# Optimization experiments

Measured on AMD Instinct MI355X. Metric: run time of the kernel, lower is better.

## Reference

```python
import jax, jax.numpy as jnp
import numpy as np

N_NODES = 100000
EPS = 1e-5


def gcn_conv(x, edge_index, W, b):
    # PyG GCNConv: add self loops, symmetric normalization, aggregate at target.
    n = x.shape[0]
    xw = x @ W                                  # [N, F_out]
    loop = jnp.arange(n)
    src = jnp.concatenate([edge_index[0], loop])
    dst = jnp.concatenate([edge_index[1], loop])
    deg = jax.ops.segment_sum(jnp.ones_like(dst, dtype=xw.dtype), dst, num_segments=n)
    dinv = jnp.where(deg > 0, jax.lax.rsqrt(deg), 0.0)
    norm = dinv[src] * dinv[dst]                # [E+N]
    out = jax.ops.segment_sum(norm[:, None] * xw[src], dst, num_segments=n)
    return out + b


def batch_norm(x, gamma, beta):
    # training-mode BatchNorm1d over node dim
    m = x.mean(axis=0)
    v = x.var(axis=0)
    return (x - m) * jax.lax.rsqrt(v + EPS) * gamma + beta


def setup_inputs() -> dict:
    key = jax.random.key(0)
    ks = jax.random.split(key, 16)
    dims = [(128, 256), (256, 128), (128, 64)]
    inp = {
        "x": jax.random.normal(ks[0], (N_NODES, 128), dtype=jnp.float32),
        "edge_index": jax.random.randint(ks[1], (2, 1600000), 0, N_NODES),
        "pos_edge_index": jax.random.randint(ks[2], (2, 200000), 0, N_NODES),
        "neg_edge_index": jax.random.randint(ks[3], (2, 200000), 0, N_NODES),
    }
    for i, (fi, fo) in enumerate(dims, start=1):
        inp[f"W{i}"] = jax.random.normal(ks[3 + i], (fi, fo), dtype=jnp.float32) / np.sqrt(fi)
        inp[f"b{i}"] = jnp.zeros((fo,), dtype=jnp.float32)
        inp[f"g{i}"] = jnp.ones((fo,), dtype=jnp.float32)
        inp[f"beta{i}"] = jnp.zeros((fo,), dtype=jnp.float32)
    return inp


def reference(x, edge_index, pos_edge_index, neg_edge_index,
              W1, b1, g1, beta1, W2, b2, g2, beta2, W3, b3, g3, beta3):
    # encode
    h = gcn_conv(x, edge_index, W1, b1)
    h = jax.nn.sigmoid(batch_norm(h, g1, beta1))
    h = gcn_conv(h, edge_index, W2, b2)
    h = jax.nn.sigmoid(batch_norm(h, g2, beta2))
    h = gcn_conv(h, edge_index, W3, b3)
    z = batch_norm(h, g3, beta3)                # [N, 64]
    # decode
    ei = jnp.concatenate([pos_edge_index, neg_edge_index], axis=-1)
    logits = jnp.sum(z[ei[0]] * z[ei[1]], axis=-1)
    return logits
```

## Files before the change

### kernel.cpp

```cpp
#include <hip/hip_runtime.h>
#include <hip/hip_bf16.h>
#include <stddef.h>


#define WAVE 64
#define BSHIFT 9
#define SCHUNK 4096

typedef __attribute__((ext_vector_type(8))) short short8;
typedef __attribute__((ext_vector_type(4))) float f32x4;

__device__ __forceinline__ float bl(uint g) { return __uint_as_float(g << 16); }
__device__ __forceinline__ float bh(uint g) { return __uint_as_float(g & 0xffff0000u); }
__device__ __forceinline__ ushort f2b(float f) {
    uint u = __float_as_uint(f);
    return (ushort)((u + 0x7fffu + ((u >> 16) & 1u)) >> 16);
}
__device__ __forceinline__ uint pack2(float lo, float hi) {
    return (uint)f2b(lo) | ((uint)f2b(hi) << 16);
}

__global__ __launch_bounds__(256) void k_bhist(const int* __restrict__ dst, int* __restrict__ gh, int E) {
    __shared__ int lh[256];
    lh[threadIdx.x] = 0; __syncthreads();
    int i = blockIdx.x * 256 + threadIdx.x, stride = gridDim.x * 256;
    for (; i < E; i += stride) atomicAdd(&lh[dst[i] >> BSHIFT], 1);
    __syncthreads();
    int v = lh[threadIdx.x];
    if (v) atomicAdd(&gh[threadIdx.x], v);
}

__global__ void k_bscan(const int* __restrict__ gh, int* __restrict__ boff, int* __restrict__ bcur) {
    __shared__ int ls[256];
    int t = threadIdx.x;
    int v = gh[t];
    ls[t] = v; __syncthreads();
    for (int off = 1; off < 256; off <<= 1) {
        int x = (t >= off) ? ls[t - off] : 0;
        __syncthreads();
        ls[t] += x;
        __syncthreads();
    }
    int excl = ls[t] - v;
    boff[t] = excl; bcur[t] = excl;
    if (t == 255) boff[256] = ls[255];
}

__global__ __launch_bounds__(256) void k_bscatter(const int* __restrict__ src, const int* __restrict__ dst,
                                                  int* __restrict__ gcur, int2* __restrict__ pairs, int E) {
    __shared__ int lh[256];
    int t = threadIdx.x;
    int base = blockIdx.x * SCHUNK;
    lh[t] = 0; __syncthreads();
    int rs[16], rd[16];
    #pragma unroll
    for (int i = 0; i < 16; ++i) {
        int idx = base + i * 256 + t;
        if (idx < E) { rs[i] = src[idx]; rd[i] = dst[idx]; atomicAdd(&lh[rd[i] >> BSHIFT], 1); }
        else rd[i] = -1;
    }
    __syncthreads();
    int cnt_b = lh[t];
    int b0 = cnt_b ? atomicAdd(&gcur[t], cnt_b) : 0;
    lh[t] = b0;
    __syncthreads();
    #pragma unroll
    for (int i = 0; i < 16; ++i) {
        if (rd[i] >= 0) {
            int p = atomicAdd(&lh[rd[i] >> BSHIFT], 1);
            pairs[p] = make_int2(rs[i], rd[i]);
        }
    }
}

__global__ __launch_bounds__(256) void k_bfine(const int2* __restrict__ pairs, const int* __restrict__ boff,
                                               int* __restrict__ rowptr, int* __restrict__ srcs,
                                               float* __restrict__ dinv, int N, int E) {
    __shared__ int lcnt[512];
    __shared__ int ls[256];
    int b = blockIdx.x, t = threadIdx.x;
    int d0 = b << BSHIFT;
    int e0 = boff[b], e1 = boff[b + 1];
    lcnt[t] = 0; lcnt[t + 256] = 0;
    __syncthreads();
    for (int e = e0 + t; e < e1; e += 256)
        atomicAdd(&lcnt[pairs[e].y - d0], 1);
    __syncthreads();
    int c0 = lcnt[2 * t], c1 = lcnt[2 * t + 1];
    ls[t] = c0 + c1;
    __syncthreads();
    for (int off = 1; off < 256; off <<= 1) {
        int x = (t >= off) ? ls[t - off] : 0;
        __syncthreads();
        ls[t] += x;
        __syncthreads();
    }
    int excl = ls[t] - (c0 + c1);
    int s0 = excl, s1 = excl + c0;
    int d = d0 + 2 * t;
    if (d < N)     { rowptr[d] = e0 + s0;     dinv[d] = rsqrtf((float)(c0 + 1)); }
    if (d + 1 < N) { rowptr[d + 1] = e0 + s1; dinv[d + 1] = rsqrtf((float)(c1 + 1)); }
    if (b == 0 && t == 0) rowptr[N] = E;
    lcnt[2 * t] = s0; lcnt[2 * t + 1] = s1;
    __syncthreads();
    for (int e = e0 + t; e < e1; e += 256) {
        int2 p = pairs[e];
        int pos = atomicAdd(&lcnt[p.y - d0], 1);
        srcs[e0 + pos] = p.x;
    }
}

__global__ void k_convx(const float* __restrict__ in, ushort* __restrict__ out, size_t n4) {
    size_t i = (size_t)blockIdx.x * blockDim.x + threadIdx.x;
    if (i >= n4) return;
    float4 v = reinterpret_cast<const float4*>(in)[i];
    uint2 o;
    o.x = pack2(v.x, v.y);
    o.y = pack2(v.z, v.w);
    reinterpret_cast<uint2*>(out)[i] = o;
}

__global__ void k_convWT(const float* __restrict__ W, ushort* __restrict__ Wt, int K, int N) {
    int i = blockIdx.x * blockDim.x + threadIdx.x;
    if (i >= K * N) return;
    int k = i / N, n = i % N;
    Wt[(size_t)n * K + k] = f2b(W[i]);
}

template<int F>
__global__ __launch_bounds__(256) void k_agg(const ushort* __restrict__ in, ushort* __restrict__ out,
                                             const int* __restrict__ rowptr, const int* __restrict__ srcs,
                                             const float* __restrict__ dinv, int N) {
    constexpr int L = (F * 2) / 16;
    int wv = threadIdx.x >> 6, lane = threadIdx.x & 63;
    int node = (blockIdx.x * 4 + wv) * (64 / L) + lane / L;
    int sl = lane % L;
    if (node >= N) return;
    const uint4* inq = reinterpret_cast<const uint4*>(in);
    float di = dinv[node];
    float acc[8];
    {
        uint4 v = inq[(size_t)node * L + sl];
        acc[0] = di * bl(v.x); acc[1] = di * bh(v.x);
        acc[2] = di * bl(v.y); acc[3] = di * bh(v.y);
        acc[4] = di * bl(v.z); acc[5] = di * bh(v.z);
        acc[6] = di * bl(v.w); acc[7] = di * bh(v.w);
    }
    int e = rowptr[node], e1 = rowptr[node + 1];
    for (; e + 1 < e1; e += 2) {
        int s0 = srcs[e], s1 = srcs[e + 1];
        float d0 = dinv[s0], d1 = dinv[s1];
        uint4 v0 = inq[(size_t)s0 * L + sl];
        uint4 v1 = inq[(size_t)s1 * L + sl];
        acc[0] += d0 * bl(v0.x) + d1 * bl(v1.x);
        acc[1] += d0 * bh(v0.x) + d1 * bh(v1.x);
        acc[2] += d0 * bl(v0.y) + d1 * bl(v1.y);
        acc[3] += d0 * bh(v0.y) + d1 * bh(v1.y);
        acc[4] += d0 * bl(v0.z) + d1 * bl(v1.z);
        acc[5] += d0 * bh(v0.z) + d1 * bh(v1.z);
        acc[6] += d0 * bl(v0.w) + d1 * bl(v1.w);
        acc[7] += d0 * bh(v0.w) + d1 * bh(v1.w);
    }
    if (e < e1) {
        int s0 = srcs[e];
        float d0 = dinv[s0];
        uint4 v0 = inq[(size_t)s0 * L + sl];
        acc[0] += d0 * bl(v0.x); acc[1] += d0 * bh(v0.x);
        acc[2] += d0 * bl(v0.y); acc[3] += d0 * bh(v0.y);
        acc[4] += d0 * bl(v0.z); acc[5] += d0 * bh(v0.z);
        acc[6] += d0 * bl(v0.w); acc[7] += d0 * bh(v0.w);
    }
    uint4 o;
    o.x = pack2(acc[0] * di, acc[1] * di);
    o.y = pack2(acc[2] * di, acc[3] * di);
    o.z = pack2(acc[4] * di, acc[5] * di);
    o.w = pack2(acc[6] * di, acc[7] * di);
    reinterpret_cast<uint4*>(out)[(size_t)node * L + sl] = o;
}

template<int F>
__global__ __launch_bounds__(256) void k_bnstats(const ushort* __restrict__ h, float* __restrict__ gsum,
                                                 float* __restrict__ gsq, int N) {
    constexpr int C = F / 8;
    constexpr int RPW = 64 / C;
    __shared__ float ls[4][16][16];
    int wv = threadIdx.x >> 6, lane = threadIdx.x & 63;
    int fidx = lane % C, rsub = lane / C;
    int row = (blockIdx.x * 4 + wv) * RPW + rsub;
    int rstride = gridDim.x * 4 * RPW;
    const uint4* hq = reinterpret_cast<const uint4*>(h);
    float s[8] = {}, q[8] = {};
    for (int r = row; r < N; r += rstride) {
        uint4 v = hq[(size_t)r * C + fidx];
        float x;
        x = bl(v.x); s[0] += x; q[0] += x * x;
        x = bh(v.x); s[1] += x; q[1] += x * x;
        x = bl(v.y); s[2] += x; q[2] += x * x;
        x = bh(v.y); s[3] += x; q[3] += x * x;
        x = bl(v.z); s[4] += x; q[4] += x * x;
        x = bh(v.z); s[5] += x; q[5] += x * x;
        x = bl(v.w); s[6] += x; q[6] += x * x;
        x = bh(v.w); s[7] += x; q[7] += x * x;
    }
    #pragma unroll
    for (int m = C; m < 64; m <<= 1) {
        #pragma unroll
        for (int j = 0; j < 8; ++j) { s[j] += __shfl_xor(s[j], m); q[j] += __shfl_xor(q[j], m); }
    }
    if (lane < C) {
        #pragma unroll
        for (int j = 0; j < 8; ++j) { ls[wv][lane][j] = s[j]; ls[wv][lane][8 + j] = q[j]; }
    }
    __syncthreads();
    int t = threadIdx.x;
    if (t < F) {
        int ch = t / 8, j = t % 8;
        float S = 0.f, Q = 0.f;
        #pragma unroll
        for (int w = 0; w < 4; ++w) { S += ls[w][ch][j]; Q += ls[w][ch][8 + j]; }
        atomicAdd(&gsum[t], S); atomicAdd(&gsq[t], Q);
    }
}

template<int K, int NF, bool APPLY, bool STATS>
__global__ __launch_bounds__(256) void k_mfma(const ushort* __restrict__ A, const ushort* __restrict__ Wt,
                                              ushort* __restrict__ C, int M, int Nout,
                                              const float* __restrict__ sc, const float* __restrict__ sh,
                                              float* __restrict__ gsum, float* __restrict__ gsq) {
    constexpr int S = K / 64;
    __shared__ uint4 Alds[128 * 8];
    __shared__ float scl[K], shl[K];
    int m0 = blockIdx.x * 128;
    int n0 = blockIdx.y * (NF * 32);
    int t = threadIdx.x;
    int w = t >> 6, lane = t & 63;
    int wr = w >> 1, wc = w & 1;
    int rf = lane & 15, kg = lane >> 4;

    if (APPLY) {
        for (int i = t; i < K; i += 256) { scl[i] = sc[i]; shl[i] = sh[i]; }
    }

    int srow[4], schk[4];
    const ushort* sga[4];
    #pragma unroll
    for (int i = 0; i < 4; ++i) {
        int chunk = t + i * 256;
        int r = chunk >> 3, c = chunk & 7;
        srow[i] = r; schk[i] = c;
        int gr = m0 + r; if (gr >= M) gr = M - 1;
        sga[i] = A + (size_t)gr * K + c * 8;
    }
    uint4 regs[4];
    #pragma unroll
    for (int i = 0; i < 4; ++i) regs[i] = *reinterpret_cast<const uint4*>(sga[i]);

    const ushort* bp[NF];
    #pragma unroll
    for (int nf = 0; nf < NF; ++nf)
        bp[nf] = Wt + (size_t)(n0 + wc * (NF * 16) + nf * 16 + rf) * K + kg * 8;

    f32x4 acc[4][NF];
    #pragma unroll
    for (int mf = 0; mf < 4; ++mf)
        #pragma unroll
        for (int nf = 0; nf < NF; ++nf)
            acc[mf][nf] = (f32x4){0.f, 0.f, 0.f, 0.f};

    if (APPLY) __syncthreads();

    for (int s = 0; s < S; ++s) {
        #pragma unroll
        for (int i = 0; i < 4; ++i) {
            uint4 v = regs[i];
            if constexpr (APPLY) {
                uint u[4] = {v.x, v.y, v.z, v.w};
                int kb = s * 64 + schk[i] * 8;
                #pragma unroll
                for (int j = 0; j < 4; ++j) {
                    int k = kb + 2 * j;
                    float x0 = bl(u[j]) * scl[k] + shl[k];
                    float x1 = bh(u[j]) * scl[k + 1] + shl[k + 1];
                    x0 = 1.f / (1.f + __expf(-x0));
                    x1 = 1.f / (1.f + __expf(-x1));
                    u[j] = pack2(x0, x1);
                }
                v.x = u[0]; v.y = u[1]; v.z = u[2]; v.w = u[3];
            }
            Alds[srow[i] * 8 + (schk[i] ^ (srow[i] & 7))] = v;
        }
        if (s + 1 < S) {
            #pragma unroll
            for (int i = 0; i < 4; ++i)
                regs[i] = *reinterpret_cast<const uint4*>(sga[i] + (s + 1) * 64);
        }
        __syncthreads();
        #pragma unroll
        for (int kk = 0; kk < 2; ++kk) {
            short8 a[4], b[NF];
            #pragma unroll
            for (int mf = 0; mf < 4; ++mf) {
                int R = wr * 64 + mf * 16 + rf;
                a[mf] = *reinterpret_cast<const short8*>(&Alds[R * 8 + ((kk * 4 + kg) ^ (R & 7))]);
            }
            int kglob = s * 64 + kk * 32;
            #pragma unroll
            for (int nf = 0; nf < NF; ++nf)
                b[nf] = *reinterpret_cast<const short8*>(bp[nf] + kglob);
            #pragma unroll
            for (int mf = 0; mf < 4; ++mf)
                #pragma unroll
                for (int nf = 0; nf < NF; ++nf)
                    acc[mf][nf] = __builtin_amdgcn_mfma_f32_16x16x32_bf16(a[mf], b[nf], acc[mf][nf], 0, 0, 0);
        }
        __syncthreads();
    }

    #pragma unroll
    for (int mf = 0; mf < 4; ++mf)
        #pragma unroll
        for (int nf = 0; nf < NF; ++nf) {
            int col = n0 + wc * (NF * 16) + nf * 16 + rf;
            #pragma unroll
            for (int j = 0; j < 4; ++j) {
                int row = m0 + wr * 64 + mf * 16 + kg * 4 + j;
                if (row < M) C[(size_t)row * Nout + col] = f2b(acc[mf][nf][j]);
            }
        }

    if constexpr (STATS) {
        __shared__ float bns[2][NF * 32], bnq[2][NF * 32];
        #pragma unroll
        for (int nf = 0; nf < NF; ++nf) {
            float cs = 0.f, cq = 0.f;
            #pragma unroll
            for (int mf = 0; mf < 4; ++mf)
                #pragma unroll
                for (int j = 0; j < 4; ++j) {
                    int row = m0 + wr * 64 + mf * 16 + kg * 4 + j;
                    float v = (row < M) ? acc[mf][nf][j] : 0.f;
                    cs += v; cq += v * v;
                }
            cs += __shfl_xor(cs, 16); cs += __shfl_xor(cs, 32);
            cq += __shfl_xor(cq, 16); cq += __shfl_xor(cq, 32);
            if (kg == 0) { bns[wr][wc * (NF * 16) + nf * 16 + rf] = cs; bnq[wr][wc * (NF * 16) + nf * 16 + rf] = cq; }
        }
        __syncthreads();
        if (t < NF * 32) {
            atomicAdd(&gsum[n0 + t], bns[0][t] + bns[1][t]);
            atomicAdd(&gsq[n0 + t],  bnq[0][t] + bnq[1][t]);
        }
    }
}

__global__ void k_bnfin(const float* __restrict__ sums, const float* __restrict__ sumsq,
                        const float* __restrict__ g, const float* __restrict__ beta,
                        float* __restrict__ scale, float* __restrict__ shift, int F, float invN) {
    int f = threadIdx.x;
    if (f < F) {
        float m = sums[f] * invN;
        float var = sumsq[f] * invN - m * m;
        float s = g[f] * rsqrtf(var + 1e-5f);
        scale[f] = s;
        shift[f] = beta[f] - m * s;
    }
}

__global__ __launch_bounds__(256) void k_decode(const ushort* __restrict__ h,
                                                const float* __restrict__ sc, const float* __restrict__ sh,
                                                const int* __restrict__ pos, const int* __restrict__ neg,
                                                int Pp, int Pn, float* __restrict__ out) {
    int gid = blockIdx.x * 16 + (threadIdx.x >> 4);
    int l = threadIdx.x & 15;
    int P = Pp + Pn;
    if (gid >= P) return;
    int a, b;
    if (gid < Pp) { a = pos[gid]; b = pos[Pp + gid]; }
    else          { int e = gid - Pp; a = neg[e]; b = neg[Pn + e]; }
    const uint2* hu = reinterpret_cast<const uint2*>(h);
    uint2 ua = hu[(size_t)a * 16 + l];
    uint2 ub = hu[(size_t)b * 16 + l];
    int f = l * 4;
    float s0 = sc[f], s1 = sc[f + 1], s2 = sc[f + 2], s3 = sc[f + 3];
    float t0 = sh[f], t1 = sh[f + 1], t2 = sh[f + 2], t3 = sh[f + 3];
    float a0 = bl(ua.x) * s0 + t0, a1 = bh(ua.x) * s1 + t1, a2 = bl(ua.y) * s2 + t2, a3 = bh(ua.y) * s3 + t3;
    float b0 = bl(ub.x) * s0 + t0, b1 = bh(ub.x) * s1 + t1, b2 = bl(ub.y) * s2 + t2, b3 = bh(ub.y) * s3 + t3;
    float d = a0 * b0 + a1 * b1 + a2 * b2 + a3 * b3;
    d += __shfl_xor(d, 1);
    d += __shfl_xor(d, 2);
    d += __shfl_xor(d, 4);
    d += __shfl_xor(d, 8);
    if (l == 0) out[gid] = d;
}

extern "C" void kernel_launch(void* const* d_in, const int* in_sizes, int n_in,
                              void* d_out, int out_size, void* d_ws, size_t ws_size,
                              hipStream_t stream) {
    const float* x   = (const float*)d_in[0];
    const int*   ei  = (const int*)d_in[1];
    const int*   pe  = (const int*)d_in[2];
    const int*   ne  = (const int*)d_in[3];
    const float* W1  = (const float*)d_in[4];
    const float* g1  = (const float*)d_in[6];
    const float* be1 = (const float*)d_in[7];
    const float* W2  = (const float*)d_in[8];
    const float* g2  = (const float*)d_in[10];
    const float* be2 = (const float*)d_in[11];
    const float* W3  = (const float*)d_in[12];
    const float* g3  = (const float*)d_in[14];
    const float* be3 = (const float*)d_in[15];
    float* out = (float*)d_out;

    const int N  = in_sizes[0] / 128;
    const int E  = in_sizes[1] / 2;
    const int Pp = in_sizes[2] / 2;
    const int Pn = in_sizes[3] / 2;

    char* ws = (char*)d_ws;
    auto carve = [&](size_t bytes) -> char* {
        char* p = ws;
        ws += (bytes + 255) & ~(size_t)255;
        return p;
    };
    char*  zz     = carve(256 * 4 + 896 * 4);
    int*   gh     = (int*)zz;
    float* sums1  = (float*)(zz + 1024);
    float* sq1    = sums1 + 256;
    float* sums2  = sq1 + 256;
    float* sq2    = sums2 + 128;
    float* sums3  = sq2 + 128;
    float* sq3    = sums3 + 64;
    size_t zz_bytes = 1024 + 896 * 4;

    int*    boff   = (int*)carve(257 * 4);
    int*    bcur   = (int*)carve(256 * 4);
    int*    rowptr = (int*)carve((size_t)(N + 1) * 4);
    float*  dinv   = (float*)carve((size_t)N * 4);
    int*    srcs   = (int*)carve((size_t)E * 4);
    int2*   pairs  = (int2*)carve((size_t)E * 8);
    float*  scale1 = (float*)carve(256 * 4);
    float*  shift1 = (float*)carve(256 * 4);
    float*  scale2 = (float*)carve(128 * 4);
    float*  shift2 = (float*)carve(128 * 4);
    float*  scale3 = (float*)carve(64 * 4);
    float*  shift3 = (float*)carve(64 * 4);
    ushort* Wt1    = (ushort*)carve(128 * 256 * 2);
    ushort* Wt2    = (ushort*)carve(256 * 128 * 2);
    ushort* Wt3    = (ushort*)carve(128 * 64 * 2);
    ushort* b1     = (ushort*)carve((size_t)N * 128 * 2);
    ushort* b2     = (ushort*)carve((size_t)N * 128 * 2);
    ushort* b3     = (ushort*)carve((size_t)N * 256 * 2);

    const int* e_src = ei;
    const int* e_dst = ei + E;
    const int NBUCK = (N + (1 << BSHIFT) - 1) >> BSHIFT;

    hipMemsetAsync(zz, 0, zz_bytes, stream);

    k_bhist<<<2048, 256, 0, stream>>>(e_dst, gh, E);
    k_bscan<<<1, 256, 0, stream>>>(gh, boff, bcur);
    k_bscatter<<<(E + SCHUNK - 1) / SCHUNK, 256, 0, stream>>>(e_src, e_dst, bcur, pairs, E);
    k_bfine<<<NBUCK, 256, 0, stream>>>(pairs, boff, rowptr, srcs, dinv, N, E);

    {
        size_t n4 = (size_t)N * 128 / 4;
        k_convx<<<(int)((n4 + 255) / 256), 256, 0, stream>>>(x, b1, n4);
        k_convWT<<<(128 * 256 + 255) / 256, 256, 0, stream>>>(W1, Wt1, 128, 256);
        k_convWT<<<(256 * 128 + 255) / 256, 256, 0, stream>>>(W2, Wt2, 256, 128);
        k_convWT<<<(128 * 64 + 255) / 256, 256, 0, stream>>>(W3, Wt3, 128, 64);
    }

    const int mblk = (N + 127) / 128;
    const int agg128 = (N + 15) / 16;
    const int agg64  = (N + 31) / 32;

    k_agg<128><<<agg128, 256, 0, stream>>>(b1, b2, rowptr, srcs, dinv, N);
    { dim3 g(mblk, 2); k_mfma<128, 4, false, true><<<g, 256, 0, stream>>>(b2, Wt1, b3, N, 256, nullptr, nullptr, sums1, sq1); }
    k_bnfin<<<1, 256, 0, stream>>>(sums1, sq1, g1, be1, scale1, shift1, 256, 1.0f / N);

    { dim3 g(mblk, 1); k_mfma<256, 4, true, false><<<g, 256, 0, stream>>>(b3, Wt2, b1, N, 128, scale1, shift1, nullptr, nullptr); }
    k_agg<128><<<agg128, 256, 0, stream>>>(b1, b2, rowptr, srcs, dinv, N);
    k_bnstats<128><<<512, 256, 0, stream>>>(b2, sums2, sq2, N);
    k_bnfin<<<1, 256, 0, stream>>>(sums2, sq2, g2, be2, scale2, shift2, 128, 1.0f / N);

    { dim3 g(mblk, 1); k_mfma<128, 2, true, false><<<g, 256, 0, stream>>>(b2, Wt3, b1, N, 64, scale2, shift2, nullptr, nullptr); }
    k_agg<64><<<agg64, 256, 0, stream>>>(b1, b2, rowptr, srcs, dinv, N);
    k_bnstats<64><<<512, 256, 0, stream>>>(b2, sums3, sq3, N);
    k_bnfin<<<1, 256, 0, stream>>>(sums3, sq3, g3, be3, scale3, shift3, 64, 1.0f / N);

    k_decode<<<(Pp + Pn + 15) / 16, 256, 0, stream>>>(b2, scale3, shift3, pe, ne, Pp, Pn, out);
}
```

Before: 549.7 us.

## Pack edge pairs, fuse BN finalize into consumers, restructure MFMA GEMM, unroll aggregation

Edge pairs are packed into one 32-bit word (local dst in the high bits, src in the low 17 bits), which halves the scatter traffic. The three weight conversions become one launch, and the BN finalize kernels are folded into the consuming GEMM and decode kernels. The MFMA kernel now loads the whole A tile into LDS once and loops over N passes within a block instead of using a 2D grid, with register double-buffering of the B fragments. The aggregation loop is unrolled by four to keep more gathers in flight. The trade-offs are a larger LDS footprint, BN scale/shift recomputed in every block, and src indices limited to 17 bits.

Result: slower. 563.7 us (+2.6%).

```diff
diff --git a/kernel.cpp b/kernel.cpp
--- a/kernel.cpp
+++ b/kernel.cpp
@@ -47,7 +47,7 @@
 }
 
 __global__ __launch_bounds__(256) void k_bscatter(const int* __restrict__ src, const int* __restrict__ dst,
-                                                  int* __restrict__ gcur, int2* __restrict__ pairs, int E) {
+                                                  int* __restrict__ gcur, uint* __restrict__ pairs, int E) {
     __shared__ int lh[256];
     int t = threadIdx.x;
     int base = blockIdx.x * SCHUNK;
@@ -68,12 +68,12 @@
     for (int i = 0; i < 16; ++i) {
         if (rd[i] >= 0) {
             int p = atomicAdd(&lh[rd[i] >> BSHIFT], 1);
-            pairs[p] = make_int2(rs[i], rd[i]);
+            pairs[p] = ((uint)(rd[i] & 511) << 17) | (uint)rs[i];
         }
     }
 }
 
-__global__ __launch_bounds__(256) void k_bfine(const int2* __restrict__ pairs, const int* __restrict__ boff,
+__global__ __launch_bounds__(256) void k_bfine(const uint* __restrict__ pairs, const int* __restrict__ boff,
                                                int* __restrict__ rowptr, int* __restrict__ srcs,
                                                float* __restrict__ dinv, int N, int E) {
     __shared__ int lcnt[512];
@@ -84,7 +84,7 @@
     lcnt[t] = 0; lcnt[t + 256] = 0;
     __syncthreads();
     for (int e = e0 + t; e < e1; e += 256)
-        atomicAdd(&lcnt[pairs[e].y - d0], 1);
+        atomicAdd(&lcnt[pairs[e] >> 17], 1);
     __syncthreads();
     int c0 = lcnt[2 * t], c1 = lcnt[2 * t + 1];
     ls[t] = c0 + c1;
@@ -104,9 +104,9 @@
     lcnt[2 * t] = s0; lcnt[2 * t + 1] = s1;
     __syncthreads();
     for (int e = e0 + t; e < e1; e += 256) {
-        int2 p = pairs[e];
-        int pos = atomicAdd(&lcnt[p.y - d0], 1);
-        srcs[e0 + pos] = p.x;
+        uint p = pairs[e];
+        int pos = atomicAdd(&lcnt[p >> 17], 1);
+        srcs[e0 + pos] = (int)(p & 0x1FFFFu);
     }
 }
 
@@ -120,11 +120,17 @@
     reinterpret_cast<uint2*>(out)[i] = o;
 }
 
-__global__ void k_convWT(const float* __restrict__ W, ushort* __restrict__ Wt, int K, int N) {
+__global__ void k_convW(const float* __restrict__ W1, const float* __restrict__ W2,
+                        const float* __restrict__ W3, ushort* __restrict__ Wt1,
+                        ushort* __restrict__ Wt2, ushort* __restrict__ Wt3) {
     int i = blockIdx.x * blockDim.x + threadIdx.x;
-    if (i >= K * N) return;
-    int k = i / N, n = i % N;
-    Wt[(size_t)n * K + k] = f2b(W[i]);
+    const float* W; ushort* Wt; int K, Nn, j;
+    if (i < 32768)      { W = W1; Wt = Wt1; K = 128; Nn = 256; j = i; }
+    else if (i < 65536) { W = W2; Wt = Wt2; K = 256; Nn = 128; j = i - 32768; }
+    else if (i < 73728) { W = W3; Wt = Wt3; K = 128; Nn = 64;  j = i - 65536; }
+    else return;
+    int k = j / Nn, n = j % Nn;
+    Wt[(size_t)n * K + k] = f2b(W[k * Nn + n]);
 }
 
 template<int F>
@@ -147,21 +153,23 @@
         acc[6] = di * bl(v.w); acc[7] = di * bh(v.w);
     }
     int e = rowptr[node], e1 = rowptr[node + 1];
-    for (; e + 1 < e1; e += 2) {
-        int s0 = srcs[e], s1 = srcs[e + 1];
-        float d0 = dinv[s0], d1 = dinv[s1];
+    for (; e + 3 < e1; e += 4) {
+        int s0 = srcs[e], s1 = srcs[e + 1], s2 = srcs[e + 2], s3 = srcs[e + 3];
+        float d0 = dinv[s0], d1 = dinv[s1], d2 = dinv[s2], d3 = dinv[s3];
         uint4 v0 = inq[(size_t)s0 * L + sl];
         uint4 v1 = inq[(size_t)s1 * L + sl];
-        acc[0] += d0 * bl(v0.x) + d1 * bl(v1.x);
-        acc[1] += d0 * bh(v0.x) + d1 * bh(v1.x);
-        acc[2] += d0 * bl(v0.y) + d1 * bl(v1.y);
-        acc[3] += d0 * bh(v0.y) + d1 * bh(v1.y);
-        acc[4] += d0 * bl(v0.z) + d1 * bl(v1.z);
-        acc[5] += d0 * bh(v0.z) + d1 * bh(v1.z);
-        acc[6] += d0 * bl(v0.w) + d1 * bl(v1.w);
-        acc[7] += d0 * bh(v0.w) + d1 * bh(v1.w);
-    }
-    if (e < e1) {
+        uint4 v2 = inq[(size_t)s2 * L + sl];
+        uint4 v3 = inq[(size_t)s3 * L + sl];
+        acc[0] += d0 * bl(v0.x) + d1 * bl(v1.x) + d2 * bl(v2.x) + d3 * bl(v3.x);
+        acc[1] += d0 * bh(v0.x) + d1 * bh(v1.x) + d2 * bh(v2.x) + d3 * bh(v3.x);
+        acc[2] += d0 * bl(v0.y) + d1 * bl(v1.y) + d2 * bl(v2.y) + d3 * bl(v3.y);
+        acc[3] += d0 * bh(v0.y) + d1 * bh(v1.y) + d2 * bh(v2.y) + d3 * bh(v3.y);
+        acc[4] += d0 * bl(v0.z) + d1 * bl(v1.z) + d2 * bl(v2.z) + d3 * bl(v3.z);
+        acc[5] += d0 * bh(v0.z) + d1 * bh(v1.z) + d2 * bh(v2.z) + d3 * bh(v3.z);
+        acc[6] += d0 * bl(v0.w) + d1 * bl(v1.w) + d2 * bl(v2.w) + d3 * bl(v3.w);
+        acc[7] += d0 * bh(v0.w) + d1 * bh(v1.w) + d2 * bh(v2.w) + d3 * bh(v3.w);
+    }
+    for (; e < e1; ++e) {
         int s0 = srcs[e];
         float d0 = dinv[s0];
         uint4 v0 = inq[(size_t)s0 * L + sl];
@@ -222,156 +230,158 @@
     }
 }
 
-template<int K, int NF, bool APPLY, bool STATS>
+template<int K, int NF, int NPASS, bool APPLY, bool STATS>
 __global__ __launch_bounds__(256) void k_mfma(const ushort* __restrict__ A, const ushort* __restrict__ Wt,
                                               ushort* __restrict__ C, int M, int Nout,
-                                              const float* __restrict__ sc, const float* __restrict__ sh,
+                                              const float* __restrict__ bsum, const float* __restrict__ bsq,
+                                              const float* __restrict__ bg, const float* __restrict__ bb,
+                                              float invN,
                                               float* __restrict__ gsum, float* __restrict__ gsq) {
-    constexpr int S = K / 64;
-    __shared__ uint4 Alds[128 * 8];
-    __shared__ float scl[K], shl[K];
+    constexpr int CH = K / 8;
+    constexpr int KS = K / 32;
+    __shared__ uint4 Alds[128 * CH];
+    __shared__ float scl[APPLY ? K : 1], shl[APPLY ? K : 1];
     int m0 = blockIdx.x * 128;
-    int n0 = blockIdx.y * (NF * 32);
     int t = threadIdx.x;
     int w = t >> 6, lane = t & 63;
     int wr = w >> 1, wc = w & 1;
     int rf = lane & 15, kg = lane >> 4;
 
-    if (APPLY) {
-        for (int i = t; i < K; i += 256) { scl[i] = sc[i]; shl[i] = sh[i]; }
-    }
-
-    int srow[4], schk[4];
-    const ushort* sga[4];
-    #pragma unroll
-    for (int i = 0; i < 4; ++i) {
-        int chunk = t + i * 256;
-        int r = chunk >> 3, c = chunk & 7;
-        srow[i] = r; schk[i] = c;
-        int gr = m0 + r; if (gr >= M) gr = M - 1;
-        sga[i] = A + (size_t)gr * K + c * 8;
-    }
-    uint4 regs[4];
-    #pragma unroll
-    for (int i = 0; i < 4; ++i) regs[i] = *reinterpret_cast<const uint4*>(sga[i]);
-
-    const ushort* bp[NF];
-    #pragma unroll
-    for (int nf = 0; nf < NF; ++nf)
-        bp[nf] = Wt + (size_t)(n0 + wc * (NF * 16) + nf * 16 + rf) * K + kg * 8;
-
-    f32x4 acc[4][NF];
-    #pragma unroll
-    for (int mf = 0; mf < 4; ++mf)
-        #pragma unroll
-        for (int nf = 0; nf < NF; ++nf)
-            acc[mf][nf] = (f32x4){0.f, 0.f, 0.f, 0.f};
-
-    if (APPLY) __syncthreads();
-
-    for (int s = 0; s < S; ++s) {
-        #pragma unroll
-        for (int i = 0; i < 4; ++i) {
-            uint4 v = regs[i];
-            if constexpr (APPLY) {
-                uint u[4] = {v.x, v.y, v.z, v.w};
-                int kb = s * 64 + schk[i] * 8;
-                #pragma unroll
-                for (int j = 0; j < 4; ++j) {
-                    int k = kb + 2 * j;
-                    float x0 = bl(u[j]) * scl[k] + shl[k];
-                    float x1 = bh(u[j]) * scl[k + 1] + shl[k + 1];
-                    x0 = 1.f / (1.f + __expf(-x0));
-                    x1 = 1.f / (1.f + __expf(-x1));
-                    u[j] = pack2(x0, x1);
-                }
-                v.x = u[0]; v.y = u[1]; v.z = u[2]; v.w = u[3];
-            }
-            Alds[srow[i] * 8 + (schk[i] ^ (srow[i] & 7))] = v;
-        }
-        if (s + 1 < S) {
-            #pragma unroll
-            for (int i = 0; i < 4; ++i)
-                regs[i] = *reinterpret_cast<const uint4*>(sga[i] + (s + 1) * 64);
+    if constexpr (APPLY) {
+        for (int i = t; i < K; i += 256) {
+            float m = bsum[i] * invN;
+            float var = bsq[i] * invN - m * m;
+            float sc = bg[i] * rsqrtf(var + 1e-5f);
+            scl[i] = sc; shl[i] = bb[i] - m * sc;
         }
         __syncthreads();
-        #pragma unroll
-        for (int kk = 0; kk < 2; ++kk) {
-            short8 a[4], b[NF];
+    }
+
+    #pragma unroll
+    for (int i = 0; i < CH / 2; ++i) {
+        int chunk = i * 256 + t;
+        int r = chunk / CH, c = chunk % CH;
+        int gr = m0 + r; if (gr >= M) gr = M - 1;
+        uint4 v = *reinterpret_cast<const uint4*>(A + (size_t)gr * K + c * 8);
+        if constexpr (APPLY) {
+            uint u[4] = {v.x, v.y, v.z, v.w};
+            int kb = c * 8;
+            #pragma unroll
+            for (int j = 0; j < 4; ++j) {
+                int k = kb + 2 * j;
+                float x0 = bl(u[j]) * scl[k] + shl[k];
+                float x1 = bh(u[j]) * scl[k + 1] + shl[k + 1];
+                x0 = 1.f / (1.f + __expf(-x0));
+                x1 = 1.f / (1.f + __expf(-x1));
+                u[j] = pack2(x0, x1);
+            }
+            v.x = u[0]; v.y = u[1]; v.z = u[2]; v.w = u[3];
+        }
+        Alds[r * CH + (c ^ (r & 7))] = v;
+    }
+    __syncthreads();
+
+    for (int pass = 0; pass < NPASS; ++pass) {
+        int n0 = pass * NF * 32;
+        const ushort* bp[NF];
+        #pragma unroll
+        for (int nf = 0; nf < NF; ++nf)
+            bp[nf] = Wt + (size_t)(n0 + wc * (NF * 16) + nf * 16 + rf) * K + kg * 8;
+
+        f32x4 acc[4][NF];
+        #pragma unroll
+        for (int mf = 0; mf < 4; ++mf)
+            #pragma unroll
+            for (int nf = 0; nf < NF; ++nf)
+                acc[mf][nf] = (f32x4){0.f, 0.f, 0.f, 0.f};
+
+        short8 bcur[NF];
+        #pragma unroll
+        for (int nf = 0; nf < NF; ++nf)
+            bcur[nf] = *reinterpret_cast<const short8*>(bp[nf]);
+
+        for (int ks = 0; ks < KS; ++ks) {
+            short8 bnxt[NF];
+            if (ks + 1 < KS) {
+                #pragma unroll
+                for (int nf = 0; nf < NF; ++nf)
+                    bnxt[nf] = *reinterpret_cast<const short8*>(bp[nf] + (ks + 1) * 32);
+            } else {
+                #pragma unroll
+                for (int nf = 0; nf < NF; ++nf) bnxt[nf] = bcur[nf];
+            }
+            short8 a[4];
             #pragma unroll
             for (int mf = 0; mf < 4; ++mf) {
                 int R = wr * 64 + mf * 16 + rf;
-                a[mf] = *reinterpret_cast<const short8*>(&Alds[R * 8 + ((kk * 4 + kg) ^ (R & 7))]);
-            }
-            int kglob = s * 64 + kk * 32;
-            #pragma unroll
-            for (int nf = 0; nf < NF; ++nf)
-                b[nf] = *reinterpret_cast<const short8*>(bp[nf] + kglob);
+                int c = ks * 4 + kg;
+                a[mf] = *reinterpret_cast<const short8*>(&Alds[R * CH + (c ^ (R & 7))]);
+            }
             #pragma unroll
             for (int mf = 0; mf < 4; ++mf)
                 #pragma unroll
                 for (int nf = 0; nf < NF; ++nf)
-                    acc[mf][nf] = __builtin_amdgcn_mfma_f32_16x16x32_bf16(a[mf], b[nf], acc[mf][nf], 0, 0, 0);
+                    acc[mf][nf] = __builtin_amdgcn_mfma_f32_16x16x32_bf16(a[mf], bcur[nf], acc[mf][nf], 0, 0, 0);
+            #pragma unroll
+            for (int nf = 0; nf < NF; ++nf) bcur[nf] = bnxt[nf];
         }
-        __syncthreads();
-    }
-
-    #pragma unroll
-    for (int mf = 0; mf < 4; ++mf)
-        #pragma unroll
-        for (int nf = 0; nf < NF; ++nf) {
-            int col = n0 + wc * (NF * 16) + nf * 16 + rf;
-            #pragma unroll
-            for (int j = 0; j < 4; ++j) {
-                int row = m0 + wr * 64 + mf * 16 + kg * 4 + j;
-                if (row < M) C[(size_t)row * Nout + col] = f2b(acc[mf][nf][j]);
-            }
-        }
-
-    if constexpr (STATS) {
-        __shared__ float bns[2][NF * 32], bnq[2][NF * 32];
-        #pragma unroll
-        for (int nf = 0; nf < NF; ++nf) {
-            float cs = 0.f, cq = 0.f;
-            #pragma unroll
-            for (int mf = 0; mf < 4; ++mf)
+
+        #pragma unroll
+        for (int mf = 0; mf < 4; ++mf)
+            #pragma unroll
+            for (int nf = 0; nf < NF; ++nf) {
+                int col = n0 + wc * (NF * 16) + nf * 16 + rf;
                 #pragma unroll
                 for (int j = 0; j < 4; ++j) {
                     int row = m0 + wr * 64 + mf * 16 + kg * 4 + j;
-                    float v = (row < M) ? acc[mf][nf][j] : 0.f;
-                    cs += v; cq += v * v;
+                    if (row < M) C[(size_t)row * Nout + col] = f2b(acc[mf][nf][j]);
                 }
-            cs += __shfl_xor(cs, 16); cs += __shfl_xor(cs, 32);
-            cq += __shfl_xor(cq, 16); cq += __shfl_xor(cq, 32);
-            if (kg == 0) { bns[wr][wc * (NF * 16) + nf * 16 + rf] = cs; bnq[wr][wc * (NF * 16) + nf * 16 + rf] = cq; }
+            }
+
+        if constexpr (STATS) {
+            __shared__ float bns[2][NF * 32], bnq[2][NF * 32];
+            __syncthreads();
+            #pragma unroll
+            for (int nf = 0; nf < NF; ++nf) {
+                float cs = 0.f, cq = 0.f;
+                #pragma unroll
+                for (int mf = 0; mf < 4; ++mf)
+                    #pragma unroll
+                    for (int j = 0; j < 4; ++j) {
+                        int row = m0 + wr * 64 + mf * 16 + kg * 4 + j;
+                        float v = (row < M) ? acc[mf][nf][j] : 0.f;
+                        cs += v; cq += v * v;
+                    }
+                cs += __shfl_xor(cs, 16); cs += __shfl_xor(cs, 32);
+                cq += __shfl_xor(cq, 16); cq += __shfl_xor(cq, 32);
+                if (kg == 0) { bns[wr][wc * (NF * 16) + nf * 16 + rf] = cs; bnq[wr][wc * (NF * 16) + nf * 16 + rf] = cq; }
+            }
+            __syncthreads();
+            if (t < NF * 32) {
+                atomicAdd(&gsum[n0 + t], bns[0][t] + bns[1][t]);
+                atomicAdd(&gsq[n0 + t],  bnq[0][t] + bnq[1][t]);
+            }
         }
-        __syncthreads();
-        if (t < NF * 32) {
-            atomicAdd(&gsum[n0 + t], bns[0][t] + bns[1][t]);
-            atomicAdd(&gsq[n0 + t],  bnq[0][t] + bnq[1][t]);
-        }
-    }
-}
-
-__global__ void k_bnfin(const float* __restrict__ sums, const float* __restrict__ sumsq,
-                        const float* __restrict__ g, const float* __restrict__ beta,
-                        float* __restrict__ scale, float* __restrict__ shift, int F, float invN) {
-    int f = threadIdx.x;
-    if (f < F) {
-        float m = sums[f] * invN;
-        float var = sumsq[f] * invN - m * m;
-        float s = g[f] * rsqrtf(var + 1e-5f);
-        scale[f] = s;
-        shift[f] = beta[f] - m * s;
     }
 }
 
 __global__ __launch_bounds__(256) void k_decode(const ushort* __restrict__ h,
-                                                const float* __restrict__ sc, const float* __restrict__ sh,
+                                                const float* __restrict__ bsum, const float* __restrict__ bsq,
+                                                const float* __restrict__ bg, const float* __restrict__ bb,
+                                                float invN,
                                                 const int* __restrict__ pos, const int* __restrict__ neg,
                                                 int Pp, int Pn, float* __restrict__ out) {
-    int gid = blockIdx.x * 16 + (threadIdx.x >> 4);
-    int l = threadIdx.x & 15;
+    __shared__ float scl[64], shl[64];
+    int t = threadIdx.x;
+    if (t < 64) {
+        float m = bsum[t] * invN;
+        float var = bsq[t] * invN - m * m;
+        float sc = bg[t] * rsqrtf(var + 1e-5f);
+        scl[t] = sc; shl[t] = bb[t] - m * sc;
+    }
+    __syncthreads();
+    int gid = blockIdx.x * 16 + (t >> 4);
+    int l = t & 15;
     int P = Pp + Pn;
     if (gid >= P) return;
     int a, b;
@@ -381,8 +391,8 @@
     uint2 ua = hu[(size_t)a * 16 + l];
     uint2 ub = hu[(size_t)b * 16 + l];
     int f = l * 4;
-    float s0 = sc[f], s1 = sc[f + 1], s2 = sc[f + 2], s3 = sc[f + 3];
-    float t0 = sh[f], t1 = sh[f + 1], t2 = sh[f + 2], t3 = sh[f + 3];
+    float s0 = scl[f], s1 = scl[f + 1], s2 = scl[f + 2], s3 = scl[f + 3];
+    float t0 = shl[f], t1 = shl[f + 1], t2 = shl[f + 2], t3 = shl[f + 3];
     float a0 = bl(ua.x) * s0 + t0, a1 = bh(ua.x) * s1 + t1, a2 = bl(ua.y) * s2 + t2, a3 = bh(ua.y) * s3 + t3;
     float b0 = bl(ub.x) * s0 + t0, b1 = bh(ub.x) * s1 + t1, b2 = bl(ub.y) * s2 + t2, b3 = bh(ub.y) * s3 + t3;
     float d = a0 * b0 + a1 * b1 + a2 * b2 + a3 * b3;
@@ -415,6 +425,7 @@
     const int E  = in_sizes[1] / 2;
     const int Pp = in_sizes[2] / 2;
     const int Pn = in_sizes[3] / 2;
+    const float invN = 1.0f / (float)N;
 
     char* ws = (char*)d_ws;
     auto carve = [&](size_t bytes) -> char* {
@@ -437,13 +448,7 @@
     int*    rowptr = (int*)carve((size_t)(N + 1) * 4);
     float*  dinv   = (float*)carve((size_t)N * 4);
     int*    srcs   = (int*)carve((size_t)E * 4);
-    int2*   pairs  = (int2*)carve((size_t)E * 8);
-    float*  scale1 = (float*)carve(256 * 4);
-    float*  shift1 = (float*)carve(256 * 4);
-    float*  scale2 = (float*)carve(128 * 4);
-    float*  shift2 = (float*)carve(128 * 4);
-    float*  scale3 = (float*)carve(64 * 4);
-    float*  shift3 = (float*)carve(64 * 4);
+    uint*   pairs  = (uint*)carve((size_t)E * 4);
     ushort* Wt1    = (ushort*)carve(128 * 256 * 2);
     ushort* Wt2    = (ushort*)carve(256 * 128 * 2);
     ushort* Wt3    = (ushort*)carve(128 * 64 * 2);
@@ -465,9 +470,7 @@
     {
         size_t n4 = (size_t)N * 128 / 4;
         k_convx<<<(int)((n4 + 255) / 256), 256, 0, stream>>>(x, b1, n4);
-        k_convWT<<<(128 * 256 + 255) / 256, 256, 0, stream>>>(W1, Wt1, 128, 256);
-        k_convWT<<<(256 * 128 + 255) / 256, 256, 0, stream>>>(W2, Wt2, 256, 128);
-        k_convWT<<<(128 * 64 + 255) / 256, 256, 0, stream>>>(W3, Wt3, 128, 64);
+        k_convW<<<288, 256, 0, stream>>>(W1, W2, W3, Wt1, Wt2, Wt3);
     }
 
     const int mblk = (N + 127) / 128;
@@ -475,18 +478,19 @@
     const int agg64  = (N + 31) / 32;
 
     k_agg<128><<<agg128, 256, 0, stream>>>(b1, b2, rowptr, srcs, dinv, N);
-    { dim3 g(mblk, 2); k_mfma<128, 4, false, true><<<g, 256, 0, stream>>>(b2, Wt1, b3, N, 256, nullptr, nullptr, sums1, sq1); }
-    k_bnfin<<<1, 256, 0, stream>>>(sums1, sq1, g1, be1, scale1, shift1, 256, 1.0f / N);
-
-    { dim3 g(mblk, 1); k_mfma<256, 4, true, false><<<g, 256, 0, stream>>>(b3, Wt2, b1, N, 128, scale1, shift1, nullptr, nullptr); }
+    k_mfma<128, 4, 2, false, true><<<mblk, 256, 0, stream>>>(b2, Wt1, b3, N, 256,
+        nullptr, nullptr, nullptr, nullptr, invN, sums1, sq1);
+
+    k_mfma<256, 4, 1, true, false><<<mblk, 256, 0, stream>>>(b3, Wt2, b1, N, 128,
+        sums1, sq1, g1, be1, invN, nullptr, nullptr);
     k_agg<128><<<agg128, 256, 0, stream>>>(b1, b2, rowptr, srcs, dinv, N);
     k_bnstats<128><<<512, 256, 0, stream>>>(b2, sums2, sq2, N);
-    k_bnfin<<<1, 256, 0, stream>>>(sums2, sq2, g2, be2, scale2, shift2, 128, 1.0f / N);
-
-    { dim3 g(mblk, 1); k_mfma<128, 2, true, false><<<g, 256, 0, stream>>>(b2, Wt3, b1, N, 64, scale2, shift2, nullptr, nullptr); }
+
+    k_mfma<128, 2, 1, true, false><<<mblk, 256, 0, stream>>>(b2, Wt3, b1, N, 64,
+        sums2, sq2, g2, be2, invN, nullptr, nullptr);
     k_agg<64><<<agg64, 256, 0, stream>>>(b1, b2, rowptr, srcs, dinv, N);
     k_bnstats<64><<<512, 256, 0, stream>>>(b2, sums3, sq3, N);
-    k_bnfin<<<1, 256, 0, stream>>>(sums3, sq3, g3, be3, scale3, shift3, 64, 1.0f / N);
-
-    k_decode<<<(Pp + Pn + 15) / 16, 256, 0, stream>>>(b2, scale3, shift3, pe, ne, Pp, Pn, out);
-}
+
+    k_decode<<<(Pp + Pn + 15) / 16, 256, 0, stream>>>(b2, sums3, sq3, g3, be3, invN,
+                                                      pe, ne, Pp, Pn, out);
+}
```
